# Kernel tuning notes

Hardware: AMD Instinct MI355X
Metric: run time of the kernel (lower is better)

Reference implementation:

```python
import jax, jax.numpy as jnp
import numpy as np

MAX_H = 512
MAX_W = 512
N_INST = 100
MASK_HW = 28


def _bilinear_sample(img, gx, gy):
    """grid_sample, mode='bilinear', padding_mode='zeros', align_corners=False.
    img: [B, H, W] float; gx, gy: [B, Ho, Wo] normalized coords in [-1, 1].
    Returns [B, Ho, Wo].
    """
    H, W = img.shape[1], img.shape[2]
    # unnormalize (align_corners=False)
    x = (gx + 1.0) * (W * 0.5) - 0.5
    y = (gy + 1.0) * (H * 0.5) - 0.5
    x0f = jnp.floor(x)
    y0f = jnp.floor(y)
    x0 = x0f.astype(jnp.int32)
    y0 = y0f.astype(jnp.int32)
    x1 = x0 + 1
    y1 = y0 + 1
    wx1 = x - x0f
    wx0 = 1.0 - wx1
    wy1 = y - y0f
    wy0 = 1.0 - wy1

    def gather(yi, xi):
        valid = (yi >= 0) & (yi < H) & (xi >= 0) & (xi < W)
        yc = jnp.clip(yi, 0, H - 1)
        xc = jnp.clip(xi, 0, W - 1)
        v = jax.vmap(lambda im, yy, xx: im[yy, xx])(img, yc, xc)
        return jnp.where(valid, v, jnp.zeros((), img.dtype))

    v00 = gather(y0, x0)
    v01 = gather(y0, x1)
    v10 = gather(y1, x0)
    v11 = gather(y1, x1)
    return (v00 * (wy0 * wx0) + v01 * (wy0 * wx1)
            + v10 * (wy1 * wx0) + v11 * (wy1 * wx1))


def setup_inputs() -> dict:
    key = jax.random.key(0)
    k1, k2, k3 = jax.random.split(key, 3)
    masks = jax.random.uniform(k1, (N_INST, 1, MASK_HW, MASK_HW), dtype=jnp.float32)
    # valid boxes inside the 512x512 canvas: x1 > x0, y1 > y0
    cxy = jax.random.uniform(k2, (N_INST, 2), minval=80.0, maxval=432.0)
    wh = jax.random.uniform(k3, (N_INST, 2), minval=32.0, maxval=256.0)
    x0y0 = jnp.clip(cxy - wh * 0.5, 0.0, MAX_W - 1.0)
    x1y1 = jnp.clip(cxy + wh * 0.5, 1.0, MAX_W - 1.0)
    boxes = jnp.concatenate([x0y0, x1y1], axis=1).astype(jnp.float32)
    return {"masks": masks, "boxes": boxes}


def reference(masks, boxes) -> jnp.ndarray:
    N, C, H, W = masks.shape
    m = masks.reshape(N * C, H, W).astype(jnp.float32)
    b = boxes.reshape(-1, 4)
    x0 = b[:, 0:1]
    y0 = b[:, 1:2]
    x1 = b[:, 2:3] + 1e-5
    y1 = b[:, 3:4] + 1e-5
    img_y = jnp.arange(MAX_H, dtype=jnp.float32) + 0.5  # [MAX_H]
    img_x = jnp.arange(MAX_W, dtype=jnp.float32) + 0.5  # [MAX_W]
    gy1d = (img_y[None, :] - y0) / (y1 - y0) * 2.0 - 1.0  # [B, MAX_H]
    gx1d = (img_x[None, :] - x0) / (x1 - x0) * 2.0 - 1.0  # [B, MAX_W]
    B = N * C
    gx = jnp.broadcast_to(gx1d[:, None, :], (B, MAX_H, MAX_W))
    gy = jnp.broadcast_to(gy1d[:, :, None], (B, MAX_H, MAX_W))
    out = _bilinear_sample(m, gx, gy)  # [B, MAX_H, MAX_W]
    return out.reshape(N, C, MAX_H, MAX_W)
```

## Files before the change

kernel.cpp:

```cpp
#include <hip/hip_runtime.h>

#define MASK_HW 28
#define OUT_H 512
#define OUT_W 512
#define N_INST 100

typedef __attribute__((ext_vector_type(4))) float f32x4;

__global__ __launch_bounds__(256) void fused_paste_kernel(
    const float* __restrict__ masks,
    const float* __restrict__ boxes,
    f32x4* __restrict__ out)
{
    const int bid = blockIdx.x;
    const int n   = bid >> 8;
    const int idx = ((bid & 255) << 8) | threadIdx.x;
    const int row = idx >> 7;
    const int xq  = idx & 127;

    f32x4* outp = out + ((size_t)n << 16) + idx;

    const float by0 = boxes[4 * n + 1];
    const float by1 = boxes[4 * n + 3] + 1e-5f;
    const float syf = 28.0f / (by1 - by0);
    const float ys  = ((float)row + 0.5f - by0) * syf - 0.5f;

    if (ys <= -1.0f || ys >= 28.0f) {
        *outp = (f32x4)0.0f;
        return;
    }

    const float bx0 = boxes[4 * n + 0];
    const float bx1 = boxes[4 * n + 2] + 1e-5f;
    const float sxf = 28.0f / (bx1 - bx0);

    const float y0f = floorf(ys);
    const int   y0i = (int)y0f;
    const float wy1 = ys - y0f;
    const float wy0 = 1.0f - wy1;
    const float wyA = (y0i >= 0)  ? wy0 : 0.0f;
    const float wyB = (y0i <= 26) ? wy1 : 0.0f;
    const int   yA  = max(y0i, 0);
    const int   yB  = min(y0i + 1, MASK_HW - 1);
    const float* mrowA = masks + (size_t)n * (MASK_HW * MASK_HW) + yA * MASK_HW;
    const float* mrowB = masks + (size_t)n * (MASK_HW * MASK_HW) + yB * MASK_HW;

    const float xbase = (float)(xq * 4) + 0.5f - bx0;
    float res[4];
    #pragma unroll
    for (int j = 0; j < 4; ++j) {
        const float xs = (xbase + (float)j) * sxf - 0.5f;
        float v = 0.0f;
        if (xs > -1.0f && xs < 28.0f) {
            const float x0f = floorf(xs);
            const int   x0i = (int)x0f;
            const float wx1 = xs - x0f;
            const float wx0 = 1.0f - wx1;
            const float wxA = (x0i >= 0)  ? wx0 : 0.0f;
            const float wxB = (x0i <= 26) ? wx1 : 0.0f;
            const int   xA  = max(x0i, 0);
            const int   xB  = min(x0i + 1, MASK_HW - 1);
            v = wyA * (wxA * mrowA[xA] + wxB * mrowA[xB]) +
                wyB * (wxA * mrowB[xA] + wxB * mrowB[xB]);
        }
        res[j] = v;
    }
    f32x4 o; o.x = res[0]; o.y = res[1]; o.z = res[2]; o.w = res[3];
    *outp = o;
}

extern "C" void kernel_launch(void* const* d_in, const int* in_sizes, int n_in,
                              void* d_out, int out_size, void* d_ws, size_t ws_size,
                              hipStream_t stream) {
    const float* masks = (const float*)d_in[0];
    const float* boxes = (const float*)d_in[1];

    fused_paste_kernel<<<dim3(N_INST * 256), dim3(256), 0, stream>>>(
        masks, boxes, (f32x4*)d_out);
}
```

Before: 117.9 us.

## Use persistent grid-stride loop with batched float4 stores over fewer blocks

Replaces the one-block-per-tile launch of 25600 blocks with 2048 blocks that loop over the output in a strided pattern. Each thread computes four float4 results, then issues their stores together, with a tail pass covering the remainder. This aims to cut block scheduling overhead and keep more stores in flight per wave. The cost is more registers per thread and less parallelism in how blocks are spread.

```diff
diff --git a/kernel.cpp b/kernel.cpp
--- a/kernel.cpp
+++ b/kernel.cpp
@@ -1,72 +1,87 @@
 #include <hip/hip_runtime.h>
 
 #define MASK_HW 28
-#define OUT_H 512
 #define OUT_W 512
 #define N_INST 100
 
 typedef __attribute__((ext_vector_type(4))) float f32x4;
+
+__device__ __forceinline__ f32x4 compute_f4(
+    const float* __restrict__ masks,
+    const float* __restrict__ boxes,
+    int idx)
+{
+    const int n   = idx >> 16;
+    const int row = (idx & 65535) >> 7;
+    const int xq  = idx & 127;
+
+    const float by0 = boxes[4 * n + 1];
+    const float by1 = boxes[4 * n + 3] + 1e-5f;
+    const float syf = 28.0f / (by1 - by0);
+    const float ys  = ((float)row + 0.5f - by0) * syf - 0.5f;
+
+    f32x4 v = (f32x4)0.0f;
+    if (ys > -1.0f && ys < 28.0f) {
+        const float bx0 = boxes[4 * n + 0];
+        const float bx1 = boxes[4 * n + 2] + 1e-5f;
+        const float sxf = 28.0f / (bx1 - bx0);
+
+        const float y0f = floorf(ys);
+        const int   y0i = (int)y0f;
+        const float wy1 = ys - y0f;
+        const float wy0 = 1.0f - wy1;
+        const float wyA = (y0i >= 0)  ? wy0 : 0.0f;
+        const float wyB = (y0i <= 26) ? wy1 : 0.0f;
+        const int   yA  = max(y0i, 0);
+        const int   yB  = min(y0i + 1, MASK_HW - 1);
+        const float* mrowA = masks + (size_t)n * (MASK_HW * MASK_HW) + yA * MASK_HW;
+        const float* mrowB = masks + (size_t)n * (MASK_HW * MASK_HW) + yB * MASK_HW;
+
+        const float xbase = (float)(xq * 4) + 0.5f - bx0;
+        #pragma unroll
+        for (int j = 0; j < 4; ++j) {
+            const float xs = (xbase + (float)j) * sxf - 0.5f;
+            float r = 0.0f;
+            if (xs > -1.0f && xs < 28.0f) {
+                const float x0f = floorf(xs);
+                const int   x0i = (int)x0f;
+                const float wx1 = xs - x0f;
+                const float wx0 = 1.0f - wx1;
+                const float wxA = (x0i >= 0)  ? wx0 : 0.0f;
+                const float wxB = (x0i <= 26) ? wx1 : 0.0f;
+                const int   xA  = max(x0i, 0);
+                const int   xB  = min(x0i + 1, MASK_HW - 1);
+                r = wyA * (wxA * mrowA[xA] + wxB * mrowA[xB]) +
+                    wyB * (wxA * mrowB[xA] + wxB * mrowB[xB]);
+            }
+            v[j] = r;
+        }
+    }
+    return v;
+}
 
 __global__ __launch_bounds__(256) void fused_paste_kernel(
     const float* __restrict__ masks,
     const float* __restrict__ boxes,
     f32x4* __restrict__ out)
 {
-    const int bid = blockIdx.x;
-    const int n   = bid >> 8;
-    const int idx = ((bid & 255) << 8) | threadIdx.x;
-    const int row = idx >> 7;
-    const int xq  = idx & 127;
+    const int gid = blockIdx.x * 256 + threadIdx.x;
+    const int S   = 2048 * 256;
 
-    f32x4* outp = out + ((size_t)n << 16) + idx;
-
-    const float by0 = boxes[4 * n + 1];
-    const float by1 = boxes[4 * n + 3] + 1e-5f;
-    const float syf = 28.0f / (by1 - by0);
-    const float ys  = ((float)row + 0.5f - by0) * syf - 0.5f;
-
-    if (ys <= -1.0f || ys >= 28.0f) {
-        *outp = (f32x4)0.0f;
-        return;
+    int i = gid;
+    for (int g = 0; g < 3; ++g) {
+        f32x4 v0 = compute_f4(masks, boxes, i);
+        f32x4 v1 = compute_f4(masks, boxes, i + S);
+        f32x4 v2 = compute_f4(masks, boxes, i + 2 * S);
+        f32x4 v3 = compute_f4(masks, boxes, i + 3 * S);
+        out[i]         = v0;
+        out[i + S]     = v1;
+        out[i + 2 * S] = v2;
+        out[i + 3 * S] = v3;
+        i += 4 * S;
     }
-
-    const float bx0 = boxes[4 * n + 0];
-    const float bx1 = boxes[4 * n + 2] + 1e-5f;
-    const float sxf = 28.0f / (bx1 - bx0);
-
-    const float y0f = floorf(ys);
-    const int   y0i = (int)y0f;
-    const float wy1 = ys - y0f;
-    const float wy0 = 1.0f - wy1;
-    const float wyA = (y0i >= 0)  ? wy0 : 0.0f;
-    const float wyB = (y0i <= 26) ? wy1 : 0.0f;
-    const int   yA  = max(y0i, 0);
-    const int   yB  = min(y0i + 1, MASK_HW - 1);
-    const float* mrowA = masks + (size_t)n * (MASK_HW * MASK_HW) + yA * MASK_HW;
-    const float* mrowB = masks + (size_t)n * (MASK_HW * MASK_HW) + yB * MASK_HW;
-
-    const float xbase = (float)(xq * 4) + 0.5f - bx0;
-    float res[4];
-    #pragma unroll
-    for (int j = 0; j < 4; ++j) {
-        const float xs = (xbase + (float)j) * sxf - 0.5f;
-        float v = 0.0f;
-        if (xs > -1.0f && xs < 28.0f) {
-            const float x0f = floorf(xs);
-            const int   x0i = (int)x0f;
-            const float wx1 = xs - x0f;
-            const float wx0 = 1.0f - wx1;
-            const float wxA = (x0i >= 0)  ? wx0 : 0.0f;
-            const float wxB = (x0i <= 26) ? wx1 : 0.0f;
-            const int   xA  = max(x0i, 0);
-            const int   xB  = min(x0i + 1, MASK_HW - 1);
-            v = wyA * (wxA * mrowA[xA] + wxB * mrowA[xB]) +
-                wyB * (wxA * mrowB[xA] + wxB * mrowB[xB]);
-        }
-        res[j] = v;
-    }
-    f32x4 o; o.x = res[0]; o.y = res[1]; o.z = res[2]; o.w = res[3];
-    *outp = o;
+    if (gid < 262144)
+        out[i] = compute_f4(masks, boxes, i);
 }
 
 extern "C" void kernel_launch(void* const* d_in, const int* in_sizes, int n_in,
@@ -75,6 +90,6 @@
     const float* masks = (const float*)d_in[0];
     const float* boxes = (const float*)d_in[1];
 
-    fused_paste_kernel<<<dim3(N_INST * 256), dim3(256), 0, stream>>>(
+    fused_paste_kernel<<<dim3(2048), dim3(256), 0, stream>>>(
         masks, boxes, (f32x4*)d_out);
 }
```

Measured after the change: 122.6 us. +4.0%, slower.
